# Kernel optimization log

Hardware: AMD Instinct MI355X
Metric: run time of the kernel (lower is better)

## Reference

```python
import jax, jax.numpy as jnp
import numpy as np


def _sparse_mask(T, S, W, G):
    """Replicates CustomSparseAttention._create_sparse_mask (bool [T, S])."""
    ii = np.arange(T)[:, None]
    jj = np.arange(S)[None, :]
    # local sliding window: cols in [i - W//2, i + W//2]
    m = (jj >= ii - W // 2) & (jj <= ii + W // 2)
    # overlapping block windows every (W - W//4) rows
    ov = W // 4
    for i in range(0, T, W - ov):
        m[i:i + W, max(0, i - ov):min(S, i + W + ov)] = True
    # strided global tokens
    if G > 0:
        stride = S // (G + 1)
        gi = np.linspace(stride, S - stride, G).astype(np.int64)  # torch .long() truncates
        m[:, gi] = True
    # diagonal +/- 1
    m |= np.abs(jj - ii) <= 1
    return jnp.asarray(m)


def setup_inputs() -> dict:
    key = jax.random.key(0)
    ks = jax.random.split(key, 8)
    B, T, S, E = 2, 2048, 2048, 512
    std = 0.02
    return {
        "query": jax.random.normal(ks[0], (B, T, E), jnp.float32),
        "key": jax.random.normal(ks[1], (B, S, E), jnp.float32),
        "value": jax.random.normal(ks[2], (B, S, E), jnp.float32),
        "Wq": jax.random.normal(ks[3], (E, E), jnp.float32) * std,
        "bq": jnp.zeros((E,), jnp.float32),
        "Wk": jax.random.normal(ks[4], (E, E), jnp.float32) * std,
        "bk": jnp.zeros((E,), jnp.float32),
        "Wv": jax.random.normal(ks[5], (E, E), jnp.float32) * std,
        "bv": jnp.zeros((E,), jnp.float32),
        "Wo": jax.random.normal(ks[6], (E, E), jnp.float32) * std,
        "bo": jnp.zeros((E,), jnp.float32),
        "temperature": jnp.ones((1,), jnp.float32) * 0.1,
        "local_window_size": 128,
        "num_global_tokens": 16,
    }


def reference(query, key, value, Wq, bq, Wk, bk, Wv, bv, Wo, bo,
              temperature, local_window_size, num_global_tokens):
    B, T, E = query.shape
    S = key.shape[1]
    H = 16
    hd = E // H
    scaling = float(hd) ** -0.5

    q = (query @ Wq.T + bq) * scaling          # [B, T, E]
    k = key @ Wk.T + bk                        # [B, S, E]
    v = value @ Wv.T + bv                      # [B, S, E]

    q = q.reshape(B, T, H, hd)
    k = k.reshape(B, S, H, hd)
    v = v.reshape(B, S, H, hd)

    # [B, H, T, S] dense scores, scaled by learned temperature
    attn = jnp.einsum('bthd,bshd->bhts', q, k) * temperature[0]

    mask = _sparse_mask(T, S, local_window_size, num_global_tokens)  # [T, S] bool
    attn = jnp.where(mask[None, None], attn, -jnp.inf)

    # (row-max subtraction in the original is the standard stable softmax)
    attn = jax.nn.softmax(attn, axis=-1)

    out = jnp.einsum('bhts,bshd->bthd', attn, v).reshape(B, T, E)
    out = out @ Wo.T + bo
    return out
```

## Files before the change

### kernel.cpp

```cpp
#include <hip/hip_runtime.h>

typedef _Float16 f16x8 __attribute__((ext_vector_type(8)));
typedef float f32x4 __attribute__((ext_vector_type(4)));

#define Tt 2048
#define Ee 512
#define Hh 16
#define HD 32
#define Bb 2
#define Mm (Bb*Tt)

__device__ __constant__ int GCOLS[16] = {120,240,361,481,602,722,843,963,
                                         1084,1204,1325,1445,1566,1686,1807,1928};

__device__ __forceinline__ int lo_of(int i) {
    int kmin = (i >= 32) ? ((i - 32) / 96) : 0;
    int lo = kmin * 96 - 32;
    return lo < 0 ? 0 : lo;
}
__device__ __forceinline__ int hi_of(int i) {
    int hi = (i / 96) * 96 + 160;
    return hi > Tt ? Tt : hi;
}

__device__ __forceinline__ f16x8 cvt8(float4 a, float4 b) {
    f16x8 r;
    r[0]=(_Float16)a.x; r[1]=(_Float16)a.y; r[2]=(_Float16)a.z; r[3]=(_Float16)a.w;
    r[4]=(_Float16)b.x; r[5]=(_Float16)b.y; r[6]=(_Float16)b.z; r[7]=(_Float16)b.w;
    return r;
}

__device__ __forceinline__ void async_copy16(const _Float16* g, _Float16* l) {
    __builtin_amdgcn_global_load_lds(
        (const __attribute__((address_space(1))) void*)g,
        (__attribute__((address_space(3))) void*)l, 16, 0, 0);
}

__global__ __launch_bounds__(256)
void cvt_kernel(const float* __restrict__ q, const float* __restrict__ k,
                const float* __restrict__ v,
                const float* __restrict__ wq, const float* __restrict__ wk,
                const float* __restrict__ wv, const float* __restrict__ wo,
                _Float16* __restrict__ dst)
{
    const int g8 = blockIdx.x * 256 + threadIdx.x;
    const float* src;
    if (g8 < 786432) {
        const int s = g8 >> 18;
        const float* xs = (s == 0) ? q : (s == 1) ? k : v;
        src = xs + (size_t)(g8 & 262143) * 8;
    } else {
        const int w8 = g8 - 786432;
        const int s = w8 >> 15;
        const float* ws = (s == 0) ? wq : (s == 1) ? wk : (s == 2) ? wv : wo;
        src = ws + (size_t)(w8 & 32767) * 8;
    }
    float4 a = ((const float4*)src)[0];
    float4 b = ((const float4*)src)[1];
    *(f16x8*)(dst + (size_t)g8 * 8) = cvt8(a, b);
}

__global__ __launch_bounds__(256)
void proj_kernel(const _Float16* __restrict__ xw,
                 const float* __restrict__ bq, const float* __restrict__ bk,
                 const float* __restrict__ bv, const float* __restrict__ temp,
                 _Float16* __restrict__ q_ws, _Float16* __restrict__ k_ws,
                 _Float16* __restrict__ v_ws)
{
    const int z = blockIdx.z;
    const _Float16* A = xw + (size_t)z * (Mm * Ee);
    const _Float16* W = xw + (size_t)3 * Mm * Ee + (size_t)z * (Ee * Ee);
    const float* bias = (z == 0) ? bq : (z == 1) ? bk : bv;

    const int m0 = blockIdx.x * 64;
    const int n0 = blockIdx.y * 128;

    __shared__ _Float16 Ash[64 * 32];
    __shared__ _Float16 Bsh[128 * 32];

    const int tid  = threadIdx.x;
    const int lane = tid & 63, wave = tid >> 6;
    const int quad = lane >> 4, l16 = lane & 15;
    const int wm = wave & 1, wn = wave >> 1;

    const int arow = tid >> 2;
    const int ac   = (tid & 3) ^ ((arow >> 1) & 3);
    const _Float16* agp  = A + (size_t)(m0 + arow) * Ee + ac * 8;
    const _Float16* bgp0 = W + (size_t)(n0 + arow) * Ee + ac * 8;
    const _Float16* bgp1 = W + (size_t)(n0 + 64 + arow) * Ee + ac * 8;
    _Float16* AshW  = Ash + wave * 512;
    _Float16* BshW0 = Bsh + wave * 512;
    _Float16* BshW1 = Bsh + 2048 + wave * 512;

    f32x4 acc[2][4] = {};

    for (int k0 = 0; k0 < Ee; k0 += 32) {
        __syncthreads();
        async_copy16(agp + k0, AshW);
        async_copy16(bgp0 + k0, BshW0);
        async_copy16(bgp1 + k0, BshW1);
        __syncthreads();

        f16x8 af[2], bf[4];
        #pragma unroll
        for (int mt = 0; mt < 2; mt++) {
            const int row = wm * 32 + mt * 16 + l16;
            af[mt] = *(const f16x8*)&Ash[row * 32 + ((quad ^ ((row >> 1) & 3)) * 8)];
        }
        #pragma unroll
        for (int nt = 0; nt < 4; nt++) {
            const int row = wn * 64 + nt * 16 + l16;
            bf[nt] = *(const f16x8*)&Bsh[row * 32 + ((quad ^ ((row >> 1) & 3)) * 8)];
        }
        #pragma unroll
        for (int mt = 0; mt < 2; mt++)
            #pragma unroll
            for (int nt = 0; nt < 4; nt++)
                acc[mt][nt] = __builtin_amdgcn_mfma_f32_16x16x32_f16(af[mt], bf[nt], acc[mt][nt], 0, 0, 0);
    }

    const float scale = (z == 0) ? (0.17677669529663687f * temp[0]) : 1.0f;
    #pragma unroll
    for (int nt = 0; nt < 4; nt++) {
        const int n = n0 + wn * 64 + nt * 16 + l16;
        const float bn = bias[n];
        const int h = n >> 5, d = n & 31;
        #pragma unroll
        for (int mt = 0; mt < 2; mt++) {
            #pragma unroll
            for (int r = 0; r < 4; r++) {
                const int m = m0 + wm * 32 + mt * 16 + quad * 4 + r;
                const float val = (acc[mt][nt][r] + bn) * scale;
                const int bidx = m >> 11, t = m & (Tt - 1);
                if (z == 2) {
                    v_ws[((size_t)(bidx * Hh + h) * HD + d) * Tt + t] = (_Float16)val;
                } else {
                    _Float16* dst = (z == 0) ? q_ws : k_ws;
                    dst[((size_t)(bidx * Hh + h) * Tt + t) * HD + d] = (_Float16)val;
                }
            }
        }
    }
}

__global__ __launch_bounds__(256)
void attn_kernel(const _Float16* __restrict__ q_ws, const _Float16* __restrict__ k_ws,
                 const _Float16* __restrict__ v_ws, _Float16* __restrict__ o_ws)
{
    const int qb = blockIdx.x * 64;
    const int h  = blockIdx.y;
    const int b  = blockIdx.z;
    const int bh = b * Hh + h;

    const int tid  = threadIdx.x;
    const int lane = tid & 63, wave = tid >> 6;
    const int quad = lane >> 4, l16 = lane & 15;
    const int t0   = qb + wave * 16;

    __shared__ _Float16 P_lds[4][16*72];
    _Float16* myP = &P_lds[wave][0];

    const f16x8 qf = *(const f16x8*)(q_ws + ((size_t)bh*Tt + t0 + l16)*HD + quad*8);

    int lo[4], hi[4];
    #pragma unroll
    for (int r = 0; r < 4; r++) {
        const int i = t0 + quad*4 + r;
        lo[r] = lo_of(i); hi[r] = hi_of(i);
    }

    float lsum[4] = {0.f, 0.f, 0.f, 0.f};
    f32x4 accO[2] = {};
    const f32x4 zf = {0.f, 0.f, 0.f, 0.f};

    {
        const int gj = GCOLS[l16];
        const f16x8 kg = *(const f16x8*)(k_ws + ((size_t)bh*Tt + gj)*HD + quad*8);
        const f32x4 s = __builtin_amdgcn_mfma_f32_16x16x32_f16(qf, kg, zf, 0, 0, 0);
        #pragma unroll
        for (int r = 0; r < 4; r++) {
            const bool inside = (gj >= lo[r]) & (gj < hi[r]);
            const float p = inside ? 0.f : __expf(s[r]);
            const _Float16 ph = (_Float16)p;
            lsum[r] += (float)ph;
            myP[(quad*4 + r)*72 + l16] = ph;
        }
        f16x8 pf;
        if (quad < 2) pf = *(const f16x8*)&myP[l16*72 + quad*8];
        else {
            #pragma unroll
            for (int j = 0; j < 8; j++) pf[j] = (_Float16)0.f;
        }
        int gck[8];
        #pragma unroll
        for (int j = 0; j < 8; j++) gck[j] = (quad < 2) ? GCOLS[quad*8 + j] : 0;
        #pragma unroll
        for (int dt = 0; dt < 2; dt++) {
            f16x8 vg;
            if (quad < 2) {
                const _Float16* vrow = v_ws + ((size_t)bh*HD + dt*16 + l16)*Tt;
                #pragma unroll
                for (int j = 0; j < 8; j++) vg[j] = vrow[gck[j]];
            } else {
                #pragma unroll
                for (int j = 0; j < 8; j++) vg[j] = (_Float16)0.f;
            }
            accO[dt] = __builtin_amdgcn_mfma_f32_16x16x32_f16(pf, vg, accO[dt], 0, 0, 0);
        }
    }

    const int cstart = lo_of(qb) & ~63;
    const int cend   = hi_of(qb + 63);
    for (int j0 = cstart; j0 < cend; j0 += 64) {
        f16x8 kf[4]; f32x4 s[4];
        #pragma unroll
        for (int nt = 0; nt < 4; nt++)
            kf[nt] = *(const f16x8*)(k_ws + ((size_t)bh*Tt + j0 + nt*16 + l16)*HD + quad*8);
        #pragma unroll
        for (int nt = 0; nt < 4; nt++)
            s[nt] = __builtin_amdgcn_mfma_f32_16x16x32_f16(qf, kf[nt], zf, 0, 0, 0);
        #pragma unroll
        for (int nt = 0; nt < 4; nt++) {
            const int j = j0 + nt*16 + l16;
            #pragma unroll
            for (int r = 0; r < 4; r++) {
                const bool inside = (j >= lo[r]) & (j < hi[r]);
                const float p = inside ? __expf(s[nt][r]) : 0.f;
                const _Float16 ph = (_Float16)p;
                lsum[r] += (float)ph;
                myP[(quad*4 + r)*72 + nt*16 + l16] = ph;
            }
        }
        #pragma unroll
        for (int kt = 0; kt < 2; kt++) {
            const f16x8 pf = *(const f16x8*)&myP[l16*72 + kt*32 + quad*8];
            #pragma unroll
            for (int dt = 0; dt < 2; dt++) {
                const f16x8 vf = *(const f16x8*)(v_ws + ((size_t)bh*HD + dt*16 + l16)*Tt
                                                 + j0 + kt*32 + quad*8);
                accO[dt] = __builtin_amdgcn_mfma_f32_16x16x32_f16(pf, vf, accO[dt], 0, 0, 0);
            }
        }
    }

    #pragma unroll
    for (int r = 0; r < 4; r++) {
        float v = lsum[r];
        v += __shfl_xor(v, 1);
        v += __shfl_xor(v, 2);
        v += __shfl_xor(v, 4);
        v += __shfl_xor(v, 8);
        lsum[r] = 1.0f / v;
    }
    #pragma unroll
    for (int dt = 0; dt < 2; dt++) {
        #pragma unroll
        for (int r = 0; r < 4; r++) {
            const int t = t0 + quad*4 + r;
            const int d = dt*16 + l16;
            o_ws[((size_t)(b*Tt + t)*Hh + h)*HD + d] = (_Float16)(accO[dt][r] * lsum[r]);
        }
    }
}

__global__ __launch_bounds__(256)
void out_kernel(const _Float16* __restrict__ Aw, const _Float16* __restrict__ Wof,
                const float* __restrict__ bo, float* __restrict__ out)
{
    const int m0 = blockIdx.x * 64;
    const int n0 = blockIdx.y * 128;

    __shared__ _Float16 Ash[64 * 32];
    __shared__ _Float16 Bsh[128 * 32];

    const int tid  = threadIdx.x;
    const int lane = tid & 63, wave = tid >> 6;
    const int quad = lane >> 4, l16 = lane & 15;
    const int wm = wave & 1, wn = wave >> 1;

    const int arow = tid >> 2;
    const int ac   = (tid & 3) ^ ((arow >> 1) & 3);
    const _Float16* agp  = Aw  + (size_t)(m0 + arow) * Ee + ac * 8;
    const _Float16* bgp0 = Wof + (size_t)(n0 + arow) * Ee + ac * 8;
    const _Float16* bgp1 = Wof + (size_t)(n0 + 64 + arow) * Ee + ac * 8;
    _Float16* AshW  = Ash + wave * 512;
    _Float16* BshW0 = Bsh + wave * 512;
    _Float16* BshW1 = Bsh + 2048 + wave * 512;

    f32x4 acc[2][4] = {};

    for (int k0 = 0; k0 < Ee; k0 += 32) {
        __syncthreads();
        async_copy16(agp + k0, AshW);
        async_copy16(bgp0 + k0, BshW0);
        async_copy16(bgp1 + k0, BshW1);
        __syncthreads();

        f16x8 af[2], bf[4];
        #pragma unroll
        for (int mt = 0; mt < 2; mt++) {
            const int row = wm * 32 + mt * 16 + l16;
            af[mt] = *(const f16x8*)&Ash[row * 32 + ((quad ^ ((row >> 1) & 3)) * 8)];
        }
        #pragma unroll
        for (int nt = 0; nt < 4; nt++) {
            const int row = wn * 64 + nt * 16 + l16;
            bf[nt] = *(const f16x8*)&Bsh[row * 32 + ((quad ^ ((row >> 1) & 3)) * 8)];
        }
        #pragma unroll
        for (int mt = 0; mt < 2; mt++)
            #pragma unroll
            for (int nt = 0; nt < 4; nt++)
                acc[mt][nt] = __builtin_amdgcn_mfma_f32_16x16x32_f16(af[mt], bf[nt], acc[mt][nt], 0, 0, 0);
    }

    #pragma unroll
    for (int nt = 0; nt < 4; nt++) {
        const int n = n0 + wn * 64 + nt * 16 + l16;
        const float bn = bo[n];
        #pragma unroll
        for (int mt = 0; mt < 2; mt++) {
            #pragma unroll
            for (int r = 0; r < 4; r++) {
                const int m = m0 + wm * 32 + mt * 16 + quad * 4 + r;
                out[(size_t)m * Ee + n] = acc[mt][nt][r] + bn;
            }
        }
    }
}

extern "C" void kernel_launch(void* const* d_in, const int* in_sizes, int n_in,
                              void* d_out, int out_size, void* d_ws, size_t ws_size,
                              hipStream_t stream)
{
    const float* query = (const float*)d_in[0];
    const float* key_  = (const float*)d_in[1];
    const float* value = (const float*)d_in[2];
    const float* Wq    = (const float*)d_in[3];
    const float* bq    = (const float*)d_in[4];
    const float* Wk    = (const float*)d_in[5];
    const float* bk    = (const float*)d_in[6];
    const float* Wv    = (const float*)d_in[7];
    const float* bv    = (const float*)d_in[8];
    const float* Wo    = (const float*)d_in[9];
    const float* bo    = (const float*)d_in[10];
    const float* temp  = (const float*)d_in[11];

    _Float16* xw   = (_Float16*)d_ws;
    _Float16* q_ws = xw + 7340032;
    _Float16* k_ws = q_ws + (size_t)Mm * Ee;
    _Float16* v_ws = k_ws + (size_t)Mm * Ee;
    _Float16* o_ws = v_ws + (size_t)Mm * Ee;
    const _Float16* Wof = xw + (size_t)3 * Mm * Ee + (size_t)3 * Ee * Ee;
    float* out = (float*)d_out;

    cvt_kernel<<<3584, 256, 0, stream>>>(query, key_, value, Wq, Wk, Wv, Wo, xw);
    proj_kernel<<<dim3(64, 4, 3), 256, 0, stream>>>(xw, bq, bk, bv, temp,
                                                    q_ws, k_ws, v_ws);
    attn_kernel<<<dim3(32, 16, 2), 256, 0, stream>>>(q_ws, k_ws, v_ws, o_ws);
    out_kernel<<<dim3(64, 4), 256, 0, stream>>>(o_ws, Wof, bo, out);
}
```

Before: 149.8 us.

## Widen GEMM K-tile to 64, narrow attention column range per wave

```diff
diff --git a/kernel.cpp b/kernel.cpp
--- a/kernel.cpp
+++ b/kernel.cpp
@@ -75,48 +75,60 @@
     const int m0 = blockIdx.x * 64;
     const int n0 = blockIdx.y * 128;
 
-    __shared__ _Float16 Ash[64 * 32];
-    __shared__ _Float16 Bsh[128 * 32];
+    __shared__ _Float16 Ash[64 * 64];
+    __shared__ _Float16 Bsh[128 * 64];
 
     const int tid  = threadIdx.x;
     const int lane = tid & 63, wave = tid >> 6;
     const int quad = lane >> 4, l16 = lane & 15;
     const int wm = wave & 1, wn = wave >> 1;
 
-    const int arow = tid >> 2;
-    const int ac   = (tid & 3) ^ ((arow >> 1) & 3);
-    const _Float16* agp  = A + (size_t)(m0 + arow) * Ee + ac * 8;
-    const _Float16* bgp0 = W + (size_t)(n0 + arow) * Ee + ac * 8;
-    const _Float16* bgp1 = W + (size_t)(n0 + 64 + arow) * Ee + ac * 8;
-    _Float16* AshW  = Ash + wave * 512;
-    _Float16* BshW0 = Bsh + wave * 512;
-    _Float16* BshW1 = Bsh + 2048 + wave * 512;
+    const int sl = lane >> 3;
+    const int lcol = ((lane & 7) ^ sl) * 8;
+    const _Float16* aSrc0 = A + (size_t)(m0 + wave*8       + sl) * Ee + lcol;
+    const _Float16* aSrc1 = A + (size_t)(m0 + (4+wave)*8   + sl) * Ee + lcol;
+    const _Float16* bSrc0 = W + (size_t)(n0 + wave*8       + sl) * Ee + lcol;
+    const _Float16* bSrc1 = W + (size_t)(n0 + (4+wave)*8   + sl) * Ee + lcol;
+    const _Float16* bSrc2 = W + (size_t)(n0 + (8+wave)*8   + sl) * Ee + lcol;
+    const _Float16* bSrc3 = W + (size_t)(n0 + (12+wave)*8  + sl) * Ee + lcol;
+    _Float16* aDst0 = Ash + wave*512;
+    _Float16* aDst1 = Ash + (4+wave)*512;
+    _Float16* bDst0 = Bsh + wave*512;
+    _Float16* bDst1 = Bsh + (4+wave)*512;
+    _Float16* bDst2 = Bsh + (8+wave)*512;
+    _Float16* bDst3 = Bsh + (12+wave)*512;
 
     f32x4 acc[2][4] = {};
 
-    for (int k0 = 0; k0 < Ee; k0 += 32) {
+    for (int k0 = 0; k0 < Ee; k0 += 64) {
         __syncthreads();
-        async_copy16(agp + k0, AshW);
-        async_copy16(bgp0 + k0, BshW0);
-        async_copy16(bgp1 + k0, BshW1);
+        async_copy16(aSrc0 + k0, aDst0);
+        async_copy16(aSrc1 + k0, aDst1);
+        async_copy16(bSrc0 + k0, bDst0);
+        async_copy16(bSrc1 + k0, bDst1);
+        async_copy16(bSrc2 + k0, bDst2);
+        async_copy16(bSrc3 + k0, bDst3);
         __syncthreads();
 
-        f16x8 af[2], bf[4];
-        #pragma unroll
-        for (int mt = 0; mt < 2; mt++) {
-            const int row = wm * 32 + mt * 16 + l16;
-            af[mt] = *(const f16x8*)&Ash[row * 32 + ((quad ^ ((row >> 1) & 3)) * 8)];
-        }
-        #pragma unroll
-        for (int nt = 0; nt < 4; nt++) {
-            const int row = wn * 64 + nt * 16 + l16;
-            bf[nt] = *(const f16x8*)&Bsh[row * 32 + ((quad ^ ((row >> 1) & 3)) * 8)];
-        }
-        #pragma unroll
-        for (int mt = 0; mt < 2; mt++)
-            #pragma unroll
-            for (int nt = 0; nt < 4; nt++)
-                acc[mt][nt] = __builtin_amdgcn_mfma_f32_16x16x32_f16(af[mt], bf[nt], acc[mt][nt], 0, 0, 0);
+        #pragma unroll
+        for (int kk = 0; kk < 2; kk++) {
+            f16x8 af[2], bf[4];
+            #pragma unroll
+            for (int mt = 0; mt < 2; mt++) {
+                const int row = wm*32 + mt*16 + l16;
+                af[mt] = *(const f16x8*)&Ash[row*64 + (((kk*4+quad) ^ (row & 7)) * 8)];
+            }
+            #pragma unroll
+            for (int nt = 0; nt < 4; nt++) {
+                const int row = wn*64 + nt*16 + l16;
+                bf[nt] = *(const f16x8*)&Bsh[row*64 + (((kk*4+quad) ^ (row & 7)) * 8)];
+            }
+            #pragma unroll
+            for (int mt = 0; mt < 2; mt++)
+                #pragma unroll
+                for (int nt = 0; nt < 4; nt++)
+                    acc[mt][nt] = __builtin_amdgcn_mfma_f32_16x16x32_f16(af[mt], bf[nt], acc[mt][nt], 0, 0, 0);
+        }
     }
 
     const float scale = (z == 0) ? (0.17677669529663687f * temp[0]) : 1.0f;
@@ -162,11 +174,11 @@
 
     const f16x8 qf = *(const f16x8*)(q_ws + ((size_t)bh*Tt + t0 + l16)*HD + quad*8);
 
-    int lo[4], hi[4];
+    int lo[4], len[4];
     #pragma unroll
     for (int r = 0; r < 4; r++) {
         const int i = t0 + quad*4 + r;
-        lo[r] = lo_of(i); hi[r] = hi_of(i);
+        lo[r] = lo_of(i); len[r] = hi_of(i) - lo[r];
     }
 
     float lsum[4] = {0.f, 0.f, 0.f, 0.f};
@@ -179,7 +191,7 @@
         const f32x4 s = __builtin_amdgcn_mfma_f32_16x16x32_f16(qf, kg, zf, 0, 0, 0);
         #pragma unroll
         for (int r = 0; r < 4; r++) {
-            const bool inside = (gj >= lo[r]) & (gj < hi[r]);
+            const bool inside = (unsigned)(gj - lo[r]) < (unsigned)len[r];
             const float p = inside ? 0.f : __expf(s[r]);
             const _Float16 ph = (_Float16)p;
             lsum[r] += (float)ph;
@@ -209,8 +221,8 @@
         }
     }
 
-    const int cstart = lo_of(qb) & ~63;
-    const int cend   = hi_of(qb + 63);
+    const int cstart = lo_of(t0) & ~63;
+    const int cend   = hi_of(t0 + 15);
     for (int j0 = cstart; j0 < cend; j0 += 64) {
         f16x8 kf[4]; f32x4 s[4];
         #pragma unroll
@@ -224,7 +236,7 @@
             const int j = j0 + nt*16 + l16;
             #pragma unroll
             for (int r = 0; r < 4; r++) {
-                const bool inside = (j >= lo[r]) & (j < hi[r]);
+                const bool inside = (unsigned)(j - lo[r]) < (unsigned)len[r];
                 const float p = inside ? __expf(s[nt][r]) : 0.f;
                 const _Float16 ph = (_Float16)p;
                 lsum[r] += (float)ph;
@@ -270,48 +282,60 @@
     const int m0 = blockIdx.x * 64;
     const int n0 = blockIdx.y * 128;
 
-    __shared__ _Float16 Ash[64 * 32];
-    __shared__ _Float16 Bsh[128 * 32];
+    __shared__ _Float16 Ash[64 * 64];
+    __shared__ _Float16 Bsh[128 * 64];
 
     const int tid  = threadIdx.x;
     const int lane = tid & 63, wave = tid >> 6;
     const int quad = lane >> 4, l16 = lane & 15;
     const int wm = wave & 1, wn = wave >> 1;
 
-    const int arow = tid >> 2;
-    const int ac   = (tid & 3) ^ ((arow >> 1) & 3);
-    const _Float16* agp  = Aw  + (size_t)(m0 + arow) * Ee + ac * 8;
-    const _Float16* bgp0 = Wof + (size_t)(n0 + arow) * Ee + ac * 8;
-    const _Float16* bgp1 = Wof + (size_t)(n0 + 64 + arow) * Ee + ac * 8;
-    _Float16* AshW  = Ash + wave * 512;
-    _Float16* BshW0 = Bsh + wave * 512;
-    _Float16* BshW1 = Bsh + 2048 + wave * 512;
+    const int sl = lane >> 3;
+    const int lcol = ((lane & 7) ^ sl) * 8;
+    const _Float16* aSrc0 = Aw  + (size_t)(m0 + wave*8      + sl) * Ee + lcol;
+    const _Float16* aSrc1 = Aw  + (size_t)(m0 + (4+wave)*8  + sl) * Ee + lcol;
+    const _Float16* bSrc0 = Wof + (size_t)(n0 + wave*8      + sl) * Ee + lcol;
+    const _Float16* bSrc1 = Wof + (size_t)(n0 + (4+wave)*8  + sl) * Ee + lcol;
+    const _Float16* bSrc2 = Wof + (size_t)(n0 + (8+wave)*8  + sl) * Ee + lcol;
+    const _Float16* bSrc3 = Wof + (size_t)(n0 + (12+wave)*8 + sl) * Ee + lcol;
+    _Float16* aDst0 = Ash + wave*512;
+    _Float16* aDst1 = Ash + (4+wave)*512;
+    _Float16* bDst0 = Bsh + wave*512;
+    _Float16* bDst1 = Bsh + (4+wave)*512;
+    _Float16* bDst2 = Bsh + (8+wave)*512;
+    _Float16* bDst3 = Bsh + (12+wave)*512;
 
     f32x4 acc[2][4] = {};
 
-    for (int k0 = 0; k0 < Ee; k0 += 32) {
+    for (int k0 = 0; k0 < Ee; k0 += 64) {
         __syncthreads();
-        async_copy16(agp + k0, AshW);
-        async_copy16(bgp0 + k0, BshW0);
-        async_copy16(bgp1 + k0, BshW1);
+        async_copy16(aSrc0 + k0, aDst0);
+        async_copy16(aSrc1 + k0, aDst1);
+        async_copy16(bSrc0 + k0, bDst0);
+        async_copy16(bSrc1 + k0, bDst1);
+        async_copy16(bSrc2 + k0, bDst2);
+        async_copy16(bSrc3 + k0, bDst3);
         __syncthreads();
 
-        f16x8 af[2], bf[4];
-        #pragma unroll
-        for (int mt = 0; mt < 2; mt++) {
-            const int row = wm * 32 + mt * 16 + l16;
-            af[mt] = *(const f16x8*)&Ash[row * 32 + ((quad ^ ((row >> 1) & 3)) * 8)];
-        }
-        #pragma unroll
-        for (int nt = 0; nt < 4; nt++) {
-            const int row = wn * 64 + nt * 16 + l16;
-            bf[nt] = *(const f16x8*)&Bsh[row * 32 + ((quad ^ ((row >> 1) & 3)) * 8)];
-        }
-        #pragma unroll
-        for (int mt = 0; mt < 2; mt++)
-            #pragma unroll
-            for (int nt = 0; nt < 4; nt++)
-                acc[mt][nt] = __builtin_amdgcn_mfma_f32_16x16x32_f16(af[mt], bf[nt], acc[mt][nt], 0, 0, 0);
+        #pragma unroll
+        for (int kk = 0; kk < 2; kk++) {
+            f16x8 af[2], bf[4];
+            #pragma unroll
+            for (int mt = 0; mt < 2; mt++) {
+                const int row = wm*32 + mt*16 + l16;
+                af[mt] = *(const f16x8*)&Ash[row*64 + (((kk*4+quad) ^ (row & 7)) * 8)];
+            }
+            #pragma unroll
+            for (int nt = 0; nt < 4; nt++) {
+                const int row = wn*64 + nt*16 + l16;
+                bf[nt] = *(const f16x8*)&Bsh[row*64 + (((kk*4+quad) ^ (row & 7)) * 8)];
+            }
+            #pragma unroll
+            for (int mt = 0; mt < 2; mt++)
+                #pragma unroll
+                for (int nt = 0; nt < 4; nt++)
+                    acc[mt][nt] = __builtin_amdgcn_mfma_f32_16x16x32_f16(af[mt], bf[nt], acc[mt][nt], 0, 0, 0);
+        }
     }
 
     #pragma unroll
```

Result: faster. 142.5 us (-4.9%).
